# Performance work log

Measured on AMD Instinct MI355X. Metric: run time of the kernel, lower is better.

The kernel has to match this reference:

```python
import jax, jax.numpy as jnp
import numpy as np

B, S, D, H = 2, 2048, 1024, 16
DK = D // H

def setup_inputs() -> dict:
    key = jax.random.key(0)
    ks = jax.random.split(key, 11)
    scale = 1.0 / np.sqrt(D)
    inp = {
        'q': jax.random.normal(ks[0], (B, S, D), jnp.float32),
        'k': jax.random.normal(ks[1], (B, S, D), jnp.float32),
        'v': jax.random.normal(ks[2], (B, S, D), jnp.float32),
        'mask': jnp.ones((1, 1, S, S), jnp.int32),
        'Wq': jax.random.normal(ks[3], (D, D), jnp.float32) * scale,
        'bq': jnp.zeros((D,), jnp.float32),
        'Wk': jax.random.normal(ks[4], (D, D), jnp.float32) * scale,
        'bk': jnp.zeros((D,), jnp.float32),
        'Wv': jax.random.normal(ks[5], (D, D), jnp.float32) * scale,
        'bv': jnp.zeros((D,), jnp.float32),
        'Wo': jax.random.normal(ks[6], (D, D), jnp.float32) * scale,
        'bo': jnp.zeros((D,), jnp.float32),
    }
    return inp

def reference(q, k, v, mask, Wq, bq, Wk, bk, Wv, bv, Wo, bo):
    # Linear projections, split into heads: [B,S,D] -> [B,H,S,DK]
    def proj(x, W, b):
        return (x @ W + b).reshape(B, -1, H, DK).transpose(0, 2, 1, 3)
    Q = proj(q, Wq, bq)
    K = proj(k, Wk, bk)
    V = proj(v, Wv, bv)
    scores = jnp.einsum('bhqd,bhkd->bhqk', Q, K) / jnp.sqrt(jnp.float32(DK))
    scores = jnp.where(mask == 0, jnp.float32(-1e9), scores)
    attn = jax.nn.softmax(scores, axis=-1)  # dropout is identity in eval mode
    out = jnp.einsum('bhqk,bhkd->bhqd', attn, V)
    out = out.transpose(0, 2, 1, 3).reshape(B, -1, D)
    return out @ Wo + bo
```

## Files before the change

kernel.cpp:

```cpp
#include <hip/hip_runtime.h>
#include <stdint.h>

#define B_  2
#define S_  2048
#define D_  1024
#define H_  16
#define M_  (B_*S_)

typedef __attribute__((ext_vector_type(8)))  short  short8;
typedef __attribute__((ext_vector_type(4)))  float  floatx4;
typedef __attribute__((ext_vector_type(16))) float  floatx16;
typedef __attribute__((ext_vector_type(4)))  float  f32x4;
typedef __attribute__((ext_vector_type(8)))  unsigned short u16x8;
typedef __attribute__((ext_vector_type(4)))  unsigned short u16x4;
typedef __attribute__((ext_vector_type(2)))  unsigned int   uint2v;

#define LOG2E_  1.44269504088896f
#define QSCALE_ (0.125f * LOG2E_)

#if __has_builtin(__builtin_amdgcn_exp2f)
  #define EXP2(x) __builtin_amdgcn_exp2f(x)
#else
  #define EXP2(x) exp2f(x)
#endif

__device__ __forceinline__ unsigned short f2bf(float x){
  union { float f; uint32_t u; } v; v.f = x;
  uint32_t r = v.u + 0x7FFFu + ((v.u >> 16) & 1u);
  return (unsigned short)(r >> 16);
}

__device__ __forceinline__ uint32_t cvt_pk_bf16(float lo, float hi){
  uint32_t r;
  asm("v_cvt_pk_bf16_f32 %0, %1, %2" : "=v"(r) : "v"(lo), "v"(hi));
  return r;
}

__device__ __forceinline__ void pl32swap(uint32_t &a, uint32_t &b){
#if __has_builtin(__builtin_amdgcn_permlane32_swap)
  uint2v r = __builtin_amdgcn_permlane32_swap(a, b, false, false);
  a = r[0]; b = r[1];
#else
  const int hi = (threadIdx.x & 63) >> 5;
  uint32_t sa = (uint32_t)__shfl_xor((int)a, 32);
  uint32_t sb = (uint32_t)__shfl_xor((int)b, 32);
  uint32_t na = hi ? sb : a;
  uint32_t nb = hi ? b  : sa;
  a = na; b = nb;
#endif
}

#define GLL16(G, L) __builtin_amdgcn_global_load_lds( \
    (const __attribute__((address_space(1))) void*)(G), \
    (__attribute__((address_space(3))) void*)(L), 16, 0, 0)

__global__ __launch_bounds__(256) void k_cvt3(const float* __restrict__ q,
        const float* __restrict__ k, const float* __restrict__ v,
        unsigned short* __restrict__ qb, unsigned short* __restrict__ kb,
        unsigned short* __restrict__ vb){
  const int z = blockIdx.y;
  const float* src = z==0 ? q : z==1 ? k : v;
  unsigned short* dst = z==0 ? qb : z==1 ? kb : vb;
  int i = blockIdx.x*256 + threadIdx.x;
  f32x4 a = ((const f32x4*)src)[i*2];
  f32x4 b = ((const f32x4*)src)[i*2+1];
  u16x8 o;
  o[0]=f2bf(a[0]); o[1]=f2bf(a[1]); o[2]=f2bf(a[2]); o[3]=f2bf(a[3]);
  o[4]=f2bf(b[0]); o[5]=f2bf(b[1]); o[6]=f2bf(b[2]); o[7]=f2bf(b[3]);
  ((u16x8*)dst)[i] = o;
}

__global__ __launch_bounds__(256) void k_wt4(const float* __restrict__ Wq,
        const float* __restrict__ Wk, const float* __restrict__ Wv, const float* __restrict__ Wo,
        unsigned short* __restrict__ wqt, unsigned short* __restrict__ wkt,
        unsigned short* __restrict__ wvt, unsigned short* __restrict__ wot){
  const int z = blockIdx.z;
  const float* W = z==0 ? Wq : z==1 ? Wk : z==2 ? Wv : Wo;
  unsigned short* Wt = z==0 ? wqt : z==1 ? wkt : z==2 ? wvt : wot;
  __shared__ float tile[32][33];
  int n0 = blockIdx.x*32, k0 = blockIdx.y*32;
  int tx = threadIdx.x, ty = threadIdx.y;
  #pragma unroll
  for (int i=0;i<32;i+=8) tile[ty+i][tx] = W[(size_t)(k0+ty+i)*D_ + n0+tx];
  __syncthreads();
  #pragma unroll
  for (int i=0;i<32;i+=8) Wt[(size_t)(n0+ty+i)*D_ + k0+tx] = f2bf(tile[tx][ty+i]);
}

__global__ __launch_bounds__(256) void k_gemm_qkv(
        const unsigned short* __restrict__ qb, const unsigned short* __restrict__ kb,
        const unsigned short* __restrict__ vb,
        const unsigned short* __restrict__ wqt, const unsigned short* __restrict__ wkt,
        const unsigned short* __restrict__ wvt,
        const float* __restrict__ bq, const float* __restrict__ bk, const float* __restrict__ bv,
        unsigned short* __restrict__ Qp, unsigned short* __restrict__ Kp,
        unsigned short* __restrict__ Vt)
{
  __shared__ __align__(16) unsigned short smem[16384];
  unsigned short* const As0 = smem;
  unsigned short* const Bs0 = smem + 4096;
  unsigned short* const As1 = smem + 8192;
  unsigned short* const Bs1 = smem + 12288;

  const int bid = blockIdx.x;
  const int xcd = bid & 7, i2 = bid >> 3;
  const int cb  = i2 & 7;
  const int p   = i2 >> 3;
  const int z   = p >> 2;
  const int row0 = (xcd + (p & 3)*8) * 128, col0 = cb * 128;

  const unsigned short* A  = z==0 ? qb  : z==1 ? kb  : vb;
  const unsigned short* Bt = z==0 ? wqt : z==1 ? wkt : wvt;
  const float* bias        = z==0 ? bq  : z==1 ? bk  : bv;

  const int tid = threadIdx.x;
  const int lane = tid & 63, wid = tid >> 6;
  const int wr = wid >> 1, wc = wid & 1;
  const int l15 = lane & 15, l4 = lane >> 4;

  floatx4 acc[4][4];
  #pragma unroll
  for (int i=0;i<4;i++)
    #pragma unroll
    for (int j=0;j<4;j++)
      #pragma unroll
      for (int r=0;r<4;r++) acc[i][j][r] = 0.f;

  auto STAGE = [&](unsigned short* As, unsigned short* Bs, int k0){
    #pragma unroll
    for (int it=0; it<2; it++){
      int idx = it*256 + tid;
      int r = idx >> 2, c = idx & 3;
      GLL16(A  + (size_t)(row0 + r)*D_ + k0 + c*8, As + (size_t)(it*4 + wid)*512);
      GLL16(Bt + (size_t)(col0 + r)*D_ + k0 + c*8, Bs + (size_t)(it*4 + wid)*512);
    }
  };
  auto COMPUTE = [&](const unsigned short* As, const unsigned short* Bs){
    short8 af[4], bfr[4];
    #pragma unroll
    for (int i=0;i<4;i++)
      af[i] = *(const short8*)(As + (wr*64 + i*16 + l15)*32 + l4*8);
    #pragma unroll
    for (int j=0;j<4;j++)
      bfr[j] = *(const short8*)(Bs + (wc*64 + j*16 + l15)*32 + l4*8);
    #pragma unroll
    for (int i=0;i<4;i++)
      #pragma unroll
      for (int j=0;j<4;j++)
        acc[i][j] = __builtin_amdgcn_mfma_f32_16x16x32_bf16(af[i], bfr[j], acc[i][j], 0,0,0);
  };

  STAGE(As0, Bs0, 0);
  __syncthreads();
  #pragma unroll 1
  for (int k0=0; k0<D_; k0+=64){
    STAGE(As1, Bs1, k0+32);
    COMPUTE(As0, Bs0);
    __syncthreads();
    if (k0 + 64 < D_) STAGE(As0, Bs0, k0+64);
    COMPUTE(As1, Bs1);
    __syncthreads();
  }

  if (z != 2){
    unsigned short* C = z==0 ? Qp : Kp;
    const float scale = z==0 ? QSCALE_ : 1.0f;
    #pragma unroll
    for (int i=0;i<4;i++){
      #pragma unroll
      for (int j=0;j<4;j++){
        int col = col0 + wc*64 + j*16 + l15;
        float bv_ = bias[col];
        int rowb = row0 + wr*64 + i*16 + l4*4;
        #pragma unroll
        for (int r=0;r<4;r++)
          C[(size_t)(rowb + r)*D_ + col] = f2bf((acc[i][j][r] + bv_) * scale);
      }
    }
  } else {
    unsigned short* tb = smem;
    const int bb = row0 >> 11, s0 = row0 & 2047;
    const int cl = wc*16 + l15;
    #pragma unroll
    for (int jp=0; jp<4; ++jp){
      __syncthreads();
      float bv_ = bias[col0 + wc*64 + jp*16 + l15];
      #pragma unroll
      for (int i=0;i<4;i++){
        u16x4 o;
        #pragma unroll
        for (int r=0;r<4;r++) o[r] = f2bf(acc[i][jp][r] + bv_);
        *(u16x4*)(tb + cl*136 + wr*64 + i*16 + l4*4) = o;
      }
      __syncthreads();
      #pragma unroll
      for (int h2=0; h2<2; ++h2){
        int slot = (tid>>4) + h2*16;
        int col  = col0 + (slot>>4)*64 + jp*16 + (slot&15);
        short8 vv = *(const short8*)(tb + slot*136 + (tid&15)*8);
        *(short8*)(Vt + ((size_t)(bb*1024 + col))*S_ + s0 + (tid&15)*8) = vv;
      }
    }
  }
}

__global__ __launch_bounds__(256) void k_gemm_out(const unsigned short* __restrict__ A,
        const unsigned short* __restrict__ Bt, const float* __restrict__ bias,
        float* __restrict__ C)
{
  __shared__ __align__(16) unsigned short smem[12288];
  unsigned short* const As0 = smem;
  unsigned short* const Bs0 = smem + 2048;
  unsigned short* const As1 = smem + 6144;
  unsigned short* const Bs1 = smem + 8192;

  const int bid = blockIdx.x;
  const int xcd = bid & 7, i2 = bid >> 3;
  const int row0 = (xcd + (i2 >> 3)*8) * 64, col0 = (i2 & 7) * 128;

  const int tid = threadIdx.x;
  const int lane = tid & 63, wid = tid >> 6;
  const int l15 = lane & 15, l4 = lane >> 4;

  floatx4 acc[4][2];
  #pragma unroll
  for (int i=0;i<4;i++)
    #pragma unroll
    for (int j=0;j<2;j++)
      #pragma unroll
      for (int r=0;r<4;r++) acc[i][j][r] = 0.f;

  auto STAGE = [&](unsigned short* As, unsigned short* Bs, int k0){
    #pragma unroll
    for (int it=0; it<2; it++){
      int idx = it*256 + tid;
      int r = idx >> 2, c = idx & 3;
      GLL16(Bt + (size_t)(col0 + r)*D_ + k0 + c*8, Bs + (size_t)(it*4 + wid)*512);
    }
    {
      int r = tid >> 2, c = tid & 3;
      GLL16(A + (size_t)(row0 + r)*D_ + k0 + c*8, As + (size_t)wid*512);
    }
  };
  auto COMPUTE = [&](const unsigned short* As, const unsigned short* Bs){
    short8 af[4], bfr[2];
    #pragma unroll
    for (int i=0;i<4;i++)
      af[i] = *(const short8*)(As + (i*16 + l15)*32 + l4*8);
    #pragma unroll
    for (int j=0;j<2;j++)
      bfr[j] = *(const short8*)(Bs + (wid*32 + j*16 + l15)*32 + l4*8);
    #pragma unroll
    for (int i=0;i<4;i++)
      #pragma unroll
      for (int j=0;j<2;j++)
        acc[i][j] = __builtin_amdgcn_mfma_f32_16x16x32_bf16(af[i], bfr[j], acc[i][j], 0,0,0);
  };

  STAGE(As0, Bs0, 0);
  __syncthreads();
  #pragma unroll 1
  for (int k0=0; k0<D_; k0+=64){
    STAGE(As1, Bs1, k0+32);
    COMPUTE(As0, Bs0);
    __syncthreads();
    if (k0 + 64 < D_) STAGE(As0, Bs0, k0+64);
    COMPUTE(As1, Bs1);
    __syncthreads();
  }

  #pragma unroll
  for (int i=0;i<4;i++){
    #pragma unroll
    for (int j=0;j<2;j++){
      int col = col0 + wid*32 + j*16 + l15;
      float bv_ = bias[col];
      int rowb = row0 + i*16 + l4*4;
      #pragma unroll
      for (int r=0;r<4;r++)
        C[(size_t)(rowb + r)*D_ + col] = acc[i][j][r] + bv_;
    }
  }
}

__global__ __launch_bounds__(256,4) void k_attn(const unsigned short* __restrict__ Qp,
        const unsigned short* __restrict__ Kp, const unsigned short* __restrict__ Vt,
        float* __restrict__ Op, float* __restrict__ Lp)
{
  __shared__ __align__(16) unsigned short smem[16384];
  unsigned short* const kb0 = smem;
  unsigned short* const vb0 = smem + 4096;
  unsigned short* const kb1 = smem + 8192;
  unsigned short* const vb1 = smem + 12288;

  const int sblk = blockIdx.x;
  const int xcd = sblk & 7, jj = sblk >> 3;
  const int bh = xcd + 8*(jj >> 5);
  const int rem = jj & 31, qt = rem >> 1, part = rem & 1;
  const int b = bh >> 4, h = bh & 15;
  const int q0 = qt*128;

  const int tid  = threadIdx.x;
  const int lane = tid & 63, wid = tid >> 6;
  const int lo5  = lane & 31, hi = lane >> 5;
  const int qm = b*S_ + q0 + wid*32 + lo5;

  short8 qf[4];
  #pragma unroll
  for (int f=0; f<4; f++)
    qf[f] = *(const short8*)(Qp + (size_t)qm*D_ + h*64 + f*16 + hi*8);

  floatx16 zv;
  #pragma unroll
  for (int r=0;r<16;r++) zv[r] = 0.f;
  floatx16 ot0 = zv, ot1 = zv;
  float lsum = 0.f;

  const int srow = tid >> 3;
  const int sc   = (tid & 7) ^ (srow & 7);
  const unsigned short* kp0 = Kp + ((size_t)b*S_)*D_ + h*64
                              + (size_t)(part*1024 + srow)*D_ + sc*8;
  const unsigned short* kp1 = kp0 + (size_t)32*D_;
  const unsigned short* vp0 = Vt + ((size_t)(b*1024 + h*64 + srow))*S_ + part*1024 + sc*8;
  const unsigned short* vp1 = vp0 + (size_t)32*S_;

  auto STAGE = [&](unsigned short* kdst, unsigned short* vdst, int tt){
    const size_t ko = (size_t)tt*64*D_;
    const int    vo = tt*64;
    GLL16(kp0 + ko, kdst + wid*512);
    GLL16(kp1 + ko, kdst + (4+wid)*512);
    GLL16(vp0 + vo, vdst + wid*512);
    GLL16(vp1 + vo, vdst + (4+wid)*512);
  };

  const int ksw = lo5 & 7;

  auto COMPUTE = [&](const unsigned short* kbuf, const unsigned short* vbuf){
    floatx16 st0, st1;
    __builtin_amdgcn_s_setprio(1);
    {
      const int cc = hi ^ ksw;
      short8 ka0 = *(const short8*)(kbuf + lo5*64      + cc*8);
      short8 ka1 = *(const short8*)(kbuf + (32+lo5)*64 + cc*8);
      st0 = __builtin_amdgcn_mfma_f32_32x32x16_bf16(ka0, qf[0], zv, 0,0,0);
      st1 = __builtin_amdgcn_mfma_f32_32x32x16_bf16(ka1, qf[0], zv, 0,0,0);
    }
    #pragma unroll
    for (int f=1; f<4; f++){
      const int cc = (2*f + hi) ^ ksw;
      short8 ka0 = *(const short8*)(kbuf + lo5*64      + cc*8);
      short8 ka1 = *(const short8*)(kbuf + (32+lo5)*64 + cc*8);
      st0 = __builtin_amdgcn_mfma_f32_32x32x16_bf16(ka0, qf[f], st0, 0,0,0);
      st1 = __builtin_amdgcn_mfma_f32_32x32x16_bf16(ka1, qf[f], st1, 0,0,0);
    }
    __builtin_amdgcn_s_setprio(0);

    #pragma unroll
    for (int kh=0; kh<2; kh++){
      const floatx16& st = kh ? st1 : st0;
      #pragma unroll
      for (int blk=0; blk<2; blk++){
        const int bs = blk*8;
        float e0 = EXP2(st[bs+0]), e1 = EXP2(st[bs+1]);
        float e2 = EXP2(st[bs+2]), e3 = EXP2(st[bs+3]);
        float e4 = EXP2(st[bs+4]), e5 = EXP2(st[bs+5]);
        float e6 = EXP2(st[bs+6]), e7 = EXP2(st[bs+7]);
        lsum += ((e0+e1)+(e2+e3)) + ((e4+e5)+(e6+e7));
        uint32_t a01 = cvt_pk_bf16(e0,e1);
        uint32_t a23 = cvt_pk_bf16(e2,e3);
        uint32_t a45 = cvt_pk_bf16(e4,e5);
        uint32_t a67 = cvt_pk_bf16(e6,e7);
        pl32swap(a01, a45);
        pl32swap(a23, a67);
        union { uint32_t w[4]; short8 v; } pu;
        pu.w[0] = a01; pu.w[1] = a23; pu.w[2] = a45; pu.w[3] = a67;
        const int kvc = kh*4 + blk*2 + hi;
        {
          const int d = lo5;
          short8 va = *(const short8*)(vbuf + d*64 + ((kvc ^ (d&7))*8));
          ot0 = __builtin_amdgcn_mfma_f32_32x32x16_bf16(va, pu.v, ot0, 0,0,0);
        }
        {
          const int d = 32 + lo5;
          short8 va = *(const short8*)(vbuf + d*64 + ((kvc ^ (d&7))*8));
          ot1 = __builtin_amdgcn_mfma_f32_32x32x16_bf16(va, pu.v, ot1, 0,0,0);
        }
      }
    }
  };

  STAGE(kb0, vb0, 0);
  __syncthreads();
  #pragma unroll 1
  for (int t2=0; t2<8; ++t2){
    const int tt = t2*2;
    STAGE(kb1, vb1, tt+1);
    COMPUTE(kb0, vb0);
    __syncthreads();
    if (t2 < 7) STAGE(kb0, vb0, tt+2);
    COMPUTE(kb1, vb1);
    __syncthreads();
  }

  lsum += __shfl_xor(lsum, 32);
  if (hi == 0)
    Lp[(size_t)part*65536 + (size_t)h*4096 + qm] = lsum;

  float* ob = Op + ((size_t)part << 22);
  #pragma unroll
  for (int r=0;r<16;r++){
    const int d = (r&3) + 8*(r>>2) + 4*hi;
    ob[(size_t)(h*64 + d)*4096      + qm] = ot0[r];
    ob[(size_t)(h*64 + d + 32)*4096 + qm] = ot1[r];
  }
}

__global__ __launch_bounds__(256) void k_combine(const float* __restrict__ Op,
        const float* __restrict__ Lp, unsigned short* __restrict__ Of)
{
  __shared__ float tile[64*68];
  __shared__ float linv[64];
  const int bx = blockIdx.x;
  const int mt = bx & 63, h = bx >> 6;
  const int m0 = mt*64, d0 = h*64;
  const int t = threadIdx.x;

  if (t < 64){
    float l0 = Lp[(size_t)h*4096 + m0 + t];
    float l1 = Lp[65536 + (size_t)h*4096 + m0 + t];
    linv[t] = 1.0f / (l0 + l1);
  }
  __syncthreads();

  const int dd = t >> 2, mc = t & 3;
  const float* p0 = Op + (size_t)(d0 + dd)*4096 + m0 + mc*16;
  const float* p1 = p0 + 4194304;
  #pragma unroll
  for (int i=0;i<4;i++){
    f32x4 a = *(const f32x4*)(p0 + i*4);
    f32x4 bb = *(const f32x4*)(p1 + i*4);
    f32x4 iv = *(const f32x4*)(linv + mc*16 + i*4);
    f32x4 vv = (a + bb) * iv;
    *(f32x4*)(tile + dd*68 + mc*16 + i*4) = vv;
  }
  __syncthreads();

  const int mm = t >> 2, dc = t & 3;
  u16x8 o0, o1;
  #pragma unroll
  for (int j=0;j<8;j++) o0[j] = f2bf(tile[(dc*16 + j)*68 + mm]);
  #pragma unroll
  for (int j=0;j<8;j++) o1[j] = f2bf(tile[(dc*16 + 8 + j)*68 + mm]);
  *(u16x8*)(Of + (size_t)(m0 + mm)*1024 + d0 + dc*16)     = o0;
  *(u16x8*)(Of + (size_t)(m0 + mm)*1024 + d0 + dc*16 + 8) = o1;
}

extern "C" void kernel_launch(void* const* d_in, const int* in_sizes, int n_in,
                              void* d_out, int out_size, void* d_ws, size_t ws_size,
                              hipStream_t stream)
{
  (void)in_sizes; (void)n_in; (void)out_size; (void)ws_size;
  const float* q  = (const float*)d_in[0];
  const float* k  = (const float*)d_in[1];
  const float* v  = (const float*)d_in[2];
  const float* Wq = (const float*)d_in[4];
  const float* bq = (const float*)d_in[5];
  const float* Wk = (const float*)d_in[6];
  const float* bk = (const float*)d_in[7];
  const float* Wv = (const float*)d_in[8];
  const float* bv = (const float*)d_in[9];
  const float* Wo = (const float*)d_in[10];
  const float* bo = (const float*)d_in[11];

  char* ws = (char*)d_ws;
  unsigned short* Qp  = (unsigned short*)(ws + 0);
  unsigned short* Kp  = (unsigned short*)(ws + 8388608);
  unsigned short* Vt  = (unsigned short*)(ws + 16777216);
  unsigned short* qb  = (unsigned short*)(ws + 25165824);
  unsigned short* kb  = (unsigned short*)(ws + 33554432);
  unsigned short* vb  = (unsigned short*)(ws + 41943040);
  unsigned short* wqt = (unsigned short*)(ws + 50331648);
  unsigned short* wkt = (unsigned short*)(ws + 52428800);
  unsigned short* wvt = (unsigned short*)(ws + 54525952);
  unsigned short* wot = (unsigned short*)(ws + 67108864);
  float*          Lp  = (float*)         (ws + 69206016);
  float*          Op  = (float*)         (ws + 33554432);
  unsigned short* Of  = qb;

  const int n8 = M_*D_/8;
  k_cvt3<<<dim3(n8/256, 3), 256, 0, stream>>>(q, k, v, qb, kb, vb);
  k_wt4<<<dim3(D_/32, D_/32, 4), dim3(32,8), 0, stream>>>(Wq, Wk, Wv, Wo,
                                                          wqt, wkt, wvt, wot);

  k_gemm_qkv<<<dim3(768), 256, 0, stream>>>(qb, kb, vb, wqt, wkt, wvt,
                                            bq, bk, bv, Qp, Kp, Vt);

  k_attn<<<dim3(1024), 256, 0, stream>>>(Qp, Kp, Vt, Op, Lp);

  k_combine<<<dim3(1024), 256, 0, stream>>>(Op, Lp, Of);

  k_gemm_out<<<dim3(512), 256, 0, stream>>>(Of, wot, bo, (float*)d_out);
}
```

Before: 130.5 us.

## Simplify QKV GEMM to single-buffered 3D grid and transpose V separately

The QKV projection GEMM drops its LDS double buffering and XCD-aware block remapping in favour of a plain 3D grid with one shared tile and two barriers per k-step. V is now written row-major into a new workspace buffer. A separate kernel then transposes it into the head-major Vt layout using a swizzled LDS tile. This simplifies the epilogue, but it adds an extra 8 MB write-and-read pass and a kernel launch, and it loses the load/compute overlap.

```diff
diff --git a/kernel.cpp b/kernel.cpp
--- a/kernel.cpp
+++ b/kernel.cpp
@@ -87,6 +87,33 @@
   for (int i=0;i<32;i+=8) Wt[(size_t)(n0+ty+i)*D_ + k0+tx] = f2bf(tile[tx][ty+i]);
 }
 
+__global__ __launch_bounds__(256) void k_vt64(const unsigned short* __restrict__ Vp,
+                                              unsigned short* __restrict__ Vt){
+  __shared__ __align__(16) unsigned short t[64*72];
+  const int tid = threadIdx.x;
+  const int col0 = blockIdx.x*64, row0 = blockIdx.y*64;
+  const int b = row0 >> 11, s0 = row0 & 2047;
+  #pragma unroll
+  for (int it=0; it<2; ++it){
+    int i = it*256 + tid;
+    int r = i >> 3, c = i & 7;
+    short8 v8 = *(const short8*)(Vp + (size_t)(row0 + r)*D_ + col0 + c*8);
+    #pragma unroll
+    for (int j=0;j<8;j++){
+      int d = c*8 + j;
+      t[d*72 + (((r>>3) ^ (d&7))*8) + (r&7)] = (unsigned short)v8[j];
+    }
+  }
+  __syncthreads();
+  #pragma unroll
+  for (int it=0; it<2; ++it){
+    int i = it*256 + tid;
+    int d = i >> 3, c = i & 7;
+    short8 v8 = *(const short8*)(t + d*72 + ((c ^ (d&7))*8));
+    *(short8*)(Vt + (size_t)(b*1024 + col0 + d)*S_ + s0 + c*8) = v8;
+  }
+}
+
 __global__ __launch_bounds__(256) void k_gemm_qkv(
         const unsigned short* __restrict__ qb, const unsigned short* __restrict__ kb,
         const unsigned short* __restrict__ vb,
@@ -94,28 +121,21 @@
         const unsigned short* __restrict__ wvt,
         const float* __restrict__ bq, const float* __restrict__ bk, const float* __restrict__ bv,
         unsigned short* __restrict__ Qp, unsigned short* __restrict__ Kp,
-        unsigned short* __restrict__ Vt)
+        unsigned short* __restrict__ Vp)
 {
-  __shared__ __align__(16) unsigned short smem[16384];
-  unsigned short* const As0 = smem;
-  unsigned short* const Bs0 = smem + 4096;
-  unsigned short* const As1 = smem + 8192;
-  unsigned short* const Bs1 = smem + 12288;
-
-  const int bid = blockIdx.x;
-  const int xcd = bid & 7, i2 = bid >> 3;
-  const int cb  = i2 & 7;
-  const int p   = i2 >> 3;
-  const int z   = p >> 2;
-  const int row0 = (xcd + (p & 3)*8) * 128, col0 = cb * 128;
-
+  __shared__ __align__(16) unsigned short As[128*32];
+  __shared__ __align__(16) unsigned short Bs[128*32];
+  const int z = blockIdx.z;
   const unsigned short* A  = z==0 ? qb  : z==1 ? kb  : vb;
   const unsigned short* Bt = z==0 ? wqt : z==1 ? wkt : wvt;
   const float* bias        = z==0 ? bq  : z==1 ? bk  : bv;
+  unsigned short* C        = z==0 ? Qp  : z==1 ? Kp  : Vp;
+  const float scale        = z==0 ? QSCALE_ : 1.0f;
 
   const int tid = threadIdx.x;
   const int lane = tid & 63, wid = tid >> 6;
   const int wr = wid >> 1, wc = wid & 1;
+  const int row0 = blockIdx.y*128, col0 = blockIdx.x*128;
   const int l15 = lane & 15, l4 = lane >> 4;
 
   floatx4 acc[4][4];
@@ -126,7 +146,8 @@
       #pragma unroll
       for (int r=0;r<4;r++) acc[i][j][r] = 0.f;
 
-  auto STAGE = [&](unsigned short* As, unsigned short* Bs, int k0){
+  for (int k0=0; k0<D_; k0+=32){
+    __syncthreads();
     #pragma unroll
     for (int it=0; it<2; it++){
       int idx = it*256 + tid;
@@ -134,8 +155,7 @@
       GLL16(A  + (size_t)(row0 + r)*D_ + k0 + c*8, As + (size_t)(it*4 + wid)*512);
       GLL16(Bt + (size_t)(col0 + r)*D_ + k0 + c*8, Bs + (size_t)(it*4 + wid)*512);
     }
-  };
-  auto COMPUTE = [&](const unsigned short* As, const unsigned short* Bs){
+    __syncthreads();
     short8 af[4], bfr[4];
     #pragma unroll
     for (int i=0;i<4;i++)
@@ -148,58 +168,18 @@
       #pragma unroll
       for (int j=0;j<4;j++)
         acc[i][j] = __builtin_amdgcn_mfma_f32_16x16x32_bf16(af[i], bfr[j], acc[i][j], 0,0,0);
-  };
-
-  STAGE(As0, Bs0, 0);
-  __syncthreads();
-  #pragma unroll 1
-  for (int k0=0; k0<D_; k0+=64){
-    STAGE(As1, Bs1, k0+32);
-    COMPUTE(As0, Bs0);
-    __syncthreads();
-    if (k0 + 64 < D_) STAGE(As0, Bs0, k0+64);
-    COMPUTE(As1, Bs1);
-    __syncthreads();
-  }
-
-  if (z != 2){
-    unsigned short* C = z==0 ? Qp : Kp;
-    const float scale = z==0 ? QSCALE_ : 1.0f;
-    #pragma unroll
-    for (int i=0;i<4;i++){
-      #pragma unroll
-      for (int j=0;j<4;j++){
-        int col = col0 + wc*64 + j*16 + l15;
-        float bv_ = bias[col];
-        int rowb = row0 + wr*64 + i*16 + l4*4;
-        #pragma unroll
-        for (int r=0;r<4;r++)
-          C[(size_t)(rowb + r)*D_ + col] = f2bf((acc[i][j][r] + bv_) * scale);
-      }
-    }
-  } else {
-    unsigned short* tb = smem;
-    const int bb = row0 >> 11, s0 = row0 & 2047;
-    const int cl = wc*16 + l15;
-    #pragma unroll
-    for (int jp=0; jp<4; ++jp){
-      __syncthreads();
-      float bv_ = bias[col0 + wc*64 + jp*16 + l15];
-      #pragma unroll
-      for (int i=0;i<4;i++){
-        u16x4 o;
-        #pragma unroll
-        for (int r=0;r<4;r++) o[r] = f2bf(acc[i][jp][r] + bv_);
-        *(u16x4*)(tb + cl*136 + wr*64 + i*16 + l4*4) = o;
-      }
-      __syncthreads();
-      #pragma unroll
-      for (int h2=0; h2<2; ++h2){
-        int slot = (tid>>4) + h2*16;
-        int col  = col0 + (slot>>4)*64 + jp*16 + (slot&15);
-        short8 vv = *(const short8*)(tb + slot*136 + (tid&15)*8);
-        *(short8*)(Vt + ((size_t)(bb*1024 + col))*S_ + s0 + (tid&15)*8) = vv;
-      }
+  }
+
+  #pragma unroll
+  for (int i=0;i<4;i++){
+    #pragma unroll
+    for (int j=0;j<4;j++){
+      int col = col0 + wc*64 + j*16 + l15;
+      float bv_ = bias[col];
+      int rowb = row0 + wr*64 + i*16 + l4*4;
+      #pragma unroll
+      for (int r=0;r<4;r++)
+        C[(size_t)(rowb + r)*D_ + col] = f2bf((acc[i][j][r] + bv_) * scale);
     }
   }
 }
@@ -482,6 +462,7 @@
   unsigned short* wqt = (unsigned short*)(ws + 50331648);
   unsigned short* wkt = (unsigned short*)(ws + 52428800);
   unsigned short* wvt = (unsigned short*)(ws + 54525952);
+  unsigned short* Vp  = (unsigned short*)(ws + 56623104);
   unsigned short* wot = (unsigned short*)(ws + 67108864);
   float*          Lp  = (float*)         (ws + 69206016);
   float*          Op  = (float*)         (ws + 33554432);
@@ -492,8 +473,10 @@
   k_wt4<<<dim3(D_/32, D_/32, 4), dim3(32,8), 0, stream>>>(Wq, Wk, Wv, Wo,
                                                           wqt, wkt, wvt, wot);
 
-  k_gemm_qkv<<<dim3(768), 256, 0, stream>>>(qb, kb, vb, wqt, wkt, wvt,
-                                            bq, bk, bv, Qp, Kp, Vt);
+  k_gemm_qkv<<<dim3(D_/128, M_/128, 3), 256, 0, stream>>>(qb, kb, vb, wqt, wkt, wvt,
+                                                          bq, bk, bv, Qp, Kp, Vp);
+
+  k_vt64<<<dim3(D_/64, M_/64), 256, 0, stream>>>(Vp, Vt);
 
   k_attn<<<dim3(1024), 256, 0, stream>>>(Qp, Kp, Vt, Op, Lp);
 
```

New measurement: 130.8 us. About the same (+0.2%).
